# Performance work log

Hardware: AMD Instinct MI355X
Metric: run time of the kernel (lower is better)

The kernel has to match this reference:

```python
import jax, jax.numpy as jnp
import numpy as np

HEADS = 4
DIM_HEAD = 64
SCALE = DIM_HEAD ** -0.5


def setup_inputs() -> dict:
    key = jax.random.key(0)
    k1, k2, k3 = jax.random.split(key, 3)
    C = 256
    hidden = HEADS * DIM_HEAD  # 256
    x = jax.random.normal(k1, (16, C, 64, 64), dtype=jnp.float32)
    # 1x1 conv weights collapsed to [out, in] matrices
    w_qkv = jax.random.normal(k2, (3 * hidden, C), dtype=jnp.float32) * (C ** -0.5)
    w_out = jax.random.normal(k3, (C, hidden), dtype=jnp.float32) * (hidden ** -0.5)
    b_out = jnp.zeros((C,), dtype=jnp.float32)
    return {"x": x, "w_qkv": w_qkv, "w_out": w_out, "b_out": b_out}


def reference(x, w_qkv, w_out, b_out):
    b, c, h, w = x.shape
    n = h * w
    # 1x1 conv == channel GEMM
    qkv = jnp.einsum('bchw,oc->bohw', x, w_qkv)           # [b, 3*hidden, h, w]
    qkv = qkv.reshape(b, 3, HEADS, DIM_HEAD, n)            # [b, 3, H, d, n]
    q, k, v = qkv[:, 0], qkv[:, 1], qkv[:, 2]              # each [b, H, d, n]
    q = jax.nn.softmax(q, axis=2) * SCALE                  # softmax over d
    k = jax.nn.softmax(k, axis=3)                          # softmax over n
    context = jnp.einsum('bhdn,bhen->bhde', k, v)          # [b, H, d, e]
    out = jnp.einsum('bhde,bhdn->bhen', context, q)        # [b, H, e, n]
    out = out.reshape(b, HEADS * DIM_HEAD, h, w)           # [b, hidden, h, w]
    return jnp.einsum('bchw,oc->bohw', out, w_out) + b_out[None, :, None, None]
```

## Files before the change

### kernel.cpp

```cpp
#include <hip/hip_runtime.h>

#define NPIX 4096
#define SCALE 0.125f

typedef _Float16 half8 __attribute__((ext_vector_type(8)));
typedef _Float16 half4 __attribute__((ext_vector_type(4)));
typedef float floatx4 __attribute__((ext_vector_type(4)));

__device__ __forceinline__ void async16(void* lds, const void* g) {
  __builtin_amdgcn_global_load_lds(
      (const __attribute__((address_space(1))) unsigned int*)(uintptr_t)g,
      (__attribute__((address_space(3))) unsigned int*)(unsigned)(uintptr_t)lds,
      16, 0, 0);
}

__global__ __launch_bounds__(256) void split16_kernel(const float* __restrict__ w,
                                                      _Float16* __restrict__ hi,
                                                      _Float16* __restrict__ lo, int n) {
  int i = blockIdx.x * 256 + threadIdx.x;
  if (i < n) {
    float v = w[i];
    _Float16 h = (_Float16)v;
    hi[i] = h;
    lo[i] = (_Float16)(v - (float)h);
  }
}

__global__ __launch_bounds__(256) void transpose16_kernel(const float* __restrict__ x,
                                                          _Float16* __restrict__ xt) {
  __shared__ float t[64][65];
  const int n0 = blockIdx.x * 64, c0 = blockIdx.y * 64, b = blockIdx.z;
  const float* xp = x + (long)b * 256 * NPIX;
  const int tid = threadIdx.x;
  const int r = tid >> 4, c4 = (tid & 15) * 4;
#pragma unroll
  for (int p = 0; p < 4; p++) {
    float4 v = *(const float4*)&xp[(long)(c0 + r + p * 16) * NPIX + n0 + c4];
    t[r + p * 16][c4 + 0] = v.x;
    t[r + p * 16][c4 + 1] = v.y;
    t[r + p * 16][c4 + 2] = v.z;
    t[r + p * 16][c4 + 3] = v.w;
  }
  __syncthreads();
  const int n = tid >> 2, cg = (tid & 3) * 16;
  alignas(16) _Float16 o[16];
#pragma unroll
  for (int i = 0; i < 16; i++) o[i] = (_Float16)t[cg + i][n];
  _Float16* dst = &xt[((long)b * NPIX + n0 + n) * 256 + c0 + cg];
  *(float4*)dst = *(float4*)&o[0];
  *(float4*)(dst + 8) = *(float4*)&o[8];
}

__global__ __launch_bounds__(256) void q_gemm_softmax(const _Float16* __restrict__ Ahp,
                                                      const _Float16* __restrict__ Alp,
                                                      const _Float16* __restrict__ Bt,
                                                      _Float16* __restrict__ PT) {
  union alignas(16) QU {
    _Float16 st[2][3][128 * 32];
    _Float16 pt[128][128];
  };
  __shared__ QU u;
  const int tid = threadIdx.x;
  const int n0 = blockIdx.x * 128, m0 = blockIdx.y * 128;
  const int bz = blockIdx.z;
  const _Float16* Bp = Bt + (long)bz * NPIX * 256;
  const int wv = tid >> 6, l = tid & 63;
  const int r16 = l & 15, q = l >> 4;
  const int mb = (wv >> 1) * 64, nb = (wv & 1) * 64;
  const int r1 = tid >> 2;
  const int o1 = ((tid & 3) * 8) ^ (((r1 >> 1) & 3) * 8);
  const int r2 = r1 + 64;
  const int ldsc1 = (wv * 64) * 8;
  const int ldsc2 = (256 + wv * 64) * 8;
  const int q8 = (q * 8) ^ (((r16 >> 1) & 3) * 8);

  auto STAGE = [&](int buf, int kt) {
    const int k0 = kt * 32;
    async16(&u.st[buf][0][ldsc1], &Ahp[(long)(m0 + r1) * 256 + k0 + o1]);
    async16(&u.st[buf][0][ldsc2], &Ahp[(long)(m0 + r2) * 256 + k0 + o1]);
    async16(&u.st[buf][1][ldsc1], &Alp[(long)(m0 + r1) * 256 + k0 + o1]);
    async16(&u.st[buf][1][ldsc2], &Alp[(long)(m0 + r2) * 256 + k0 + o1]);
    async16(&u.st[buf][2][ldsc1], &Bp[(long)(n0 + r1) * 256 + k0 + o1]);
    async16(&u.st[buf][2][ldsc2], &Bp[(long)(n0 + r2) * 256 + k0 + o1]);
  };

  floatx4 acc[4][4];
#pragma unroll
  for (int i = 0; i < 4; i++)
#pragma unroll
    for (int j = 0; j < 4; j++) acc[i][j] = (floatx4){0.f, 0.f, 0.f, 0.f};

  STAGE(0, 0);
  __syncthreads();
  int cur = 0;
  for (int kt = 0; kt < 8; kt++) {
    if (kt < 7) STAGE(cur ^ 1, kt + 1);
    half8 fa[4], flo[4], fb[4];
#pragma unroll
    for (int i = 0; i < 4; i++) {
      fa[i] = *(const half8*)&u.st[cur][0][(mb + i * 16 + r16) * 32 + q8];
      flo[i] = *(const half8*)&u.st[cur][1][(mb + i * 16 + r16) * 32 + q8];
      fb[i] = *(const half8*)&u.st[cur][2][(nb + i * 16 + r16) * 32 + q8];
    }
#pragma unroll
    for (int i = 0; i < 4; i++)
#pragma unroll
      for (int j = 0; j < 4; j++) {
        acc[i][j] = __builtin_amdgcn_mfma_f32_16x16x32_f16(fa[i], fb[j], acc[i][j], 0, 0, 0);
        acc[i][j] = __builtin_amdgcn_mfma_f32_16x16x32_f16(flo[i], fb[j], acc[i][j], 0, 0, 0);
      }
    __syncthreads();
    cur ^= 1;
  }

#pragma unroll
  for (int j = 0; j < 4; j++) {
    float s = 0.f;
#pragma unroll
    for (int i = 0; i < 4; i++)
#pragma unroll
      for (int t = 0; t < 4; t++) {
        float e = __expf(acc[i][j][t]);
        acc[i][j][t] = e;
        s += e;
      }
    s += __shfl_xor(s, 16, 64);
    s += __shfl_xor(s, 32, 64);
    const float rinv = 1.0f / s;
    const int nl = nb + j * 16 + r16;
    const int swz = (nl & 7) * 8;
#pragma unroll
    for (int i = 0; i < 4; i++) {
      half4 h4;
#pragma unroll
      for (int t = 0; t < 4; t++) h4[t] = (_Float16)(acc[i][j][t] * rinv);
      *(half4*)&u.pt[nl][(mb + i * 16 + q * 4) ^ swz] = h4;
    }
  }
  __syncthreads();
  const int rbase = tid >> 4, c16 = tid & 15;
  _Float16* dst = PT + ((long)(bz * 2 + (m0 >> 7)) * NPIX + n0) * 128;
#pragma unroll
  for (int k = 0; k < 8; k++) {
    const int row = rbase + k * 16;
    const int chunk = c16 ^ (row & 7);
    float4 v = *(const float4*)&u.pt[row][chunk * 8];
    *(float4*)&dst[(long)row * 128 + c16 * 8] = v;
  }
}

#define CPB 2
__global__ __launch_bounds__(256) void kv_ctx_gemm(const _Float16* __restrict__ Ahp,
                                                   const _Float16* __restrict__ Alp,
                                                   const _Float16* __restrict__ Bt,
                                                   float* __restrict__ pbuf,
                                                   float* __restrict__ rsbuf) {
  union alignas(16) KVU {
    _Float16 st[2][3][128 * 32];
    _Float16 ev[128][136];
  };
  __shared__ KVU u;
  const int tid = threadIdx.x;
  const int cg = blockIdx.x;
  const int hi = blockIdx.y;
  const int b = blockIdx.z;
  const _Float16* Bp = Bt + (long)b * NPIX * 256;
  const int wv = tid >> 6, l = tid & 63;
  const int r16 = l & 15, q = l >> 4;
  const int mb = (wv >> 1) * 64, nb = (wv & 1) * 64;
  const int r1 = tid >> 2;
  const int o1 = ((tid & 3) * 8) ^ (((r1 >> 1) & 3) * 8);
  const int ldsc1 = (wv * 64) * 8;
  const int ldsc2 = (256 + wv * 64) * 8;
  const int q8 = (q * 8) ^ (((r16 >> 1) & 3) * 8);
  const long gAk = (long)(256 + hi * 64 + r1) * 256;
  const long gAv = (long)(512 + hi * 64 + r1) * 256;

  auto STAGE = [&](int buf, int kt, int n0) {
    const int k0 = kt * 32;
    async16(&u.st[buf][0][ldsc1], &Ahp[gAk + k0 + o1]);
    async16(&u.st[buf][0][ldsc2], &Ahp[gAv + k0 + o1]);
    async16(&u.st[buf][1][ldsc1], &Alp[gAk + k0 + o1]);
    async16(&u.st[buf][1][ldsc2], &Alp[gAv + k0 + o1]);
    async16(&u.st[buf][2][ldsc1], &Bp[(long)(n0 + r1) * 256 + k0 + o1]);
    async16(&u.st[buf][2][ldsc2], &Bp[(long)(n0 + 64 + r1) * 256 + k0 + o1]);
  };

  floatx4 c2[4];
#pragma unroll
  for (int j = 0; j < 4; j++) c2[j] = (floatx4){0.f, 0.f, 0.f, 0.f};
  float rs = 0.f;

  for (int cs = 0; cs < CPB; cs++) {
    const int n0 = (cg * CPB + cs) * 128;
    floatx4 acc[4][4];
#pragma unroll
    for (int i = 0; i < 4; i++)
#pragma unroll
      for (int j = 0; j < 4; j++) acc[i][j] = (floatx4){0.f, 0.f, 0.f, 0.f};

    STAGE(0, 0, n0);
    __syncthreads();
    int cur = 0;
    for (int kt = 0; kt < 8; kt++) {
      if (kt < 7) STAGE(cur ^ 1, kt + 1, n0);
      half8 fa[4], flo[4], fb[4];
#pragma unroll
      for (int i = 0; i < 4; i++) {
        fa[i] = *(const half8*)&u.st[cur][0][(mb + i * 16 + r16) * 32 + q8];
        flo[i] = *(const half8*)&u.st[cur][1][(mb + i * 16 + r16) * 32 + q8];
        fb[i] = *(const half8*)&u.st[cur][2][(nb + i * 16 + r16) * 32 + q8];
      }
#pragma unroll
      for (int i = 0; i < 4; i++)
#pragma unroll
        for (int j = 0; j < 4; j++) {
          acc[i][j] = __builtin_amdgcn_mfma_f32_16x16x32_f16(fa[i], fb[j], acc[i][j], 0, 0, 0);
          acc[i][j] = __builtin_amdgcn_mfma_f32_16x16x32_f16(flo[i], fb[j], acc[i][j], 0, 0, 0);
        }
      __syncthreads();
      cur ^= 1;
    }

    const bool is_k = (mb == 0);
#pragma unroll
    for (int i = 0; i < 4; i++) {
      const int row = mb + i * 16 + q * 4;
#pragma unroll
      for (int j = 0; j < 4; j++) {
        const int col = nb + j * 16 + r16;
#pragma unroll
        for (int t = 0; t < 4; t++) {
          const float vv0 = acc[i][j][t];
          u.ev[row + t][col] = (_Float16)(is_k ? __expf(vv0) : vv0);
        }
      }
    }
    __syncthreads();

#pragma unroll
    for (int ks = 0; ks < 4; ks++) {
      half8 a = *(const half8*)&u.ev[wv * 16 + r16][ks * 32 + q * 8];
#pragma unroll
      for (int ii = 0; ii < 8; ii++) rs += (float)a[ii];
#pragma unroll
      for (int j = 0; j < 4; j++) {
        half8 bv = *(const half8*)&u.ev[64 + j * 16 + r16][ks * 32 + q * 8];
        c2[j] = __builtin_amdgcn_mfma_f32_16x16x32_f16(a, bv, c2[j], 0, 0, 0);
      }
    }
    __syncthreads();
  }

  rs += __shfl_xor(rs, 16, 64);
  rs += __shfl_xor(rs, 32, 64);
  const int bh = b * 4 + hi;
  float* pp = pbuf + ((long)bh * 16 + cg) * 4096;
#pragma unroll
  for (int j = 0; j < 4; j++)
#pragma unroll
    for (int reg = 0; reg < 4; reg++)
      pp[(wv * 16 + q * 4 + reg) * 64 + j * 16 + r16] = c2[j][reg];
  if (l < 16) rsbuf[((long)bh * 16 + cg) * 64 + wv * 16 + r16] = rs;
}

__global__ __launch_bounds__(256) void reduce_ctx(const float* __restrict__ pbuf,
                                                  float* __restrict__ ctx) {
  int g = blockIdx.x * 256 + threadIdx.x;
  int bh = g >> 12, e = g & 4095;
  const float* pp = pbuf + ((long)bh * 16) * 4096 + e;
  float s = 0.f;
#pragma unroll
  for (int c = 0; c < 16; c++) s += pp[(long)c * 4096];
  ctx[g] = s;
}

__global__ __launch_bounds__(256) void zinv_kernel(const float* __restrict__ rsbuf,
                                                   float* __restrict__ kinvz) {
  int g = blockIdx.x * 256 + threadIdx.x;
  int bh = g >> 6, d = g & 63;
  const float* rp = rsbuf + (long)bh * 16 * 64 + d;
  float s = 0.f;
#pragma unroll
  for (int c = 0; c < 16; c++) s += rp[c * 64];
  kinvz[g] = 1.0f / s;
}

__global__ __launch_bounds__(256) void mctx_kernel(const float* __restrict__ w_out,
                                                   const float* __restrict__ ctx,
                                                   const float* __restrict__ kinvz,
                                                   _Float16* __restrict__ Mhi,
                                                   _Float16* __restrict__ Mlo) {
  __shared__ float sctxT[64][65];
  const int cq = blockIdx.x, h = blockIdx.y, b = blockIdx.z;
  const int bh = b * 4 + h;
  const float* cp = ctx + (long)bh * 4096;
  const int tid = threadIdx.x;
  {
    const int d = tid >> 2, e0 = (tid & 3) * 16;
#pragma unroll
    for (int k = 0; k < 4; k++) {
      float4 v = *(const float4*)&cp[d * 64 + e0 + k * 4];
      sctxT[e0 + k * 4 + 0][d] = v.x;
      sctxT[e0 + k * 4 + 1][d] = v.y;
      sctxT[e0 + k * 4 + 2][d] = v.z;
      sctxT[e0 + k * 4 + 3][d] = v.w;
    }
  }
  __syncthreads();
  const int c = cq * 64 + (tid >> 2);
  const int d0 = (tid & 3) * 16;
  const float* wp = w_out + (long)c * 256 + h * 64;
  float acc[16];
#pragma unroll
  for (int i = 0; i < 16; i++) acc[i] = 0.f;
#pragma unroll
  for (int e4 = 0; e4 < 16; e4++) {
    float4 wv = *(const float4*)&wp[e4 * 4];
#pragma unroll
    for (int u2 = 0; u2 < 4; u2++) {
      const float we = ((const float*)&wv)[u2];
      const int e = e4 * 4 + u2;
#pragma unroll
      for (int dd = 0; dd < 16; dd++) acc[dd] = fmaf(we, sctxT[e][d0 + dd], acc[dd]);
    }
  }
  alignas(16) _Float16 hi16[16], lo16[16];
#pragma unroll
  for (int k4 = 0; k4 < 4; k4++) {
    float4 zv = *(const float4*)&kinvz[bh * 64 + d0 + k4 * 4];
#pragma unroll
    for (int u2 = 0; u2 < 4; u2++) {
      const int dd = k4 * 4 + u2;
      float v = acc[dd] * (SCALE * ((const float*)&zv)[u2]);
      _Float16 hh = (_Float16)v;
      hi16[dd] = hh;
      lo16[dd] = (_Float16)(v - (float)hh);
    }
  }
  _Float16* mh = Mhi + ((long)b * 256 + c) * 256 + h * 64 + d0;
  _Float16* ml = Mlo + ((long)b * 256 + c) * 256 + h * 64 + d0;
#pragma unroll
  for (int k = 0; k < 2; k++) {
    *(float4*)&mh[k * 8] = *(float4*)&hi16[k * 8];
    *(float4*)&ml[k * 8] = *(float4*)&lo16[k * 8];
  }
}

__global__ __launch_bounds__(256) void out_gemm(const _Float16* __restrict__ Mhi,
                                                const _Float16* __restrict__ Mlo,
                                                const _Float16* __restrict__ PT,
                                                float* __restrict__ C,
                                                const float* __restrict__ bias) {
  __shared__ _Float16 st[2][3][128 * 32];
  const int tid = threadIdx.x;
  const int n0 = blockIdx.x * 128, m0 = blockIdx.y * 128;
  const int b = blockIdx.z;
  const _Float16* Ah = Mhi + (long)b * 65536;
  const _Float16* Al = Mlo + (long)b * 65536;
  float* Cp = C + (long)b * 256 * NPIX;
  const int wv = tid >> 6, l = tid & 63;
  const int r16 = l & 15, q = l >> 4;
  const int mb = (wv >> 1) * 64, nb = (wv & 1) * 64;
  const int r1 = tid >> 2;
  const int o1 = ((tid & 3) * 8) ^ (((r1 >> 1) & 3) * 8);
  const int r2 = r1 + 64;
  const int ldsc1 = (wv * 64) * 8;
  const int ldsc2 = (256 + wv * 64) * 8;
  const int q8 = (q * 8) ^ (((r16 >> 1) & 3) * 8);

  auto STAGE = [&](int buf, int kt) {
    const int k0 = kt * 32;
    async16(&st[buf][0][ldsc1], &Ah[(long)(m0 + r1) * 256 + k0 + o1]);
    async16(&st[buf][0][ldsc2], &Ah[(long)(m0 + r2) * 256 + k0 + o1]);
    async16(&st[buf][1][ldsc1], &Al[(long)(m0 + r1) * 256 + k0 + o1]);
    async16(&st[buf][1][ldsc2], &Al[(long)(m0 + r2) * 256 + k0 + o1]);
    const _Float16* Bk = PT + ((long)(b * 2 + (kt >> 2)) * NPIX + n0) * 128;
    async16(&st[buf][2][ldsc1], &Bk[(long)r1 * 128 + (kt & 3) * 32 + o1]);
    async16(&st[buf][2][ldsc2], &Bk[(long)(r1 + 64) * 128 + (kt & 3) * 32 + o1]);
  };

  floatx4 acc[4][4];
#pragma unroll
  for (int i = 0; i < 4; i++)
#pragma unroll
    for (int j = 0; j < 4; j++) acc[i][j] = (floatx4){0.f, 0.f, 0.f, 0.f};

  STAGE(0, 0);
  __syncthreads();
  int cur = 0;
  for (int kt = 0; kt < 8; kt++) {
    if (kt < 7) STAGE(cur ^ 1, kt + 1);
    half8 fa[4], flo[4], fb[4];
#pragma unroll
    for (int i = 0; i < 4; i++) {
      fa[i] = *(const half8*)&st[cur][0][(mb + i * 16 + r16) * 32 + q8];
      flo[i] = *(const half8*)&st[cur][1][(mb + i * 16 + r16) * 32 + q8];
      fb[i] = *(const half8*)&st[cur][2][(nb + i * 16 + r16) * 32 + q8];
    }
#pragma unroll
    for (int i = 0; i < 4; i++)
#pragma unroll
      for (int j = 0; j < 4; j++) {
        acc[i][j] = __builtin_amdgcn_mfma_f32_16x16x32_f16(fa[i], fb[j], acc[i][j], 0, 0, 0);
        acc[i][j] = __builtin_amdgcn_mfma_f32_16x16x32_f16(flo[i], fb[j], acc[i][j], 0, 0, 0);
      }
    __syncthreads();
    cur ^= 1;
  }
#pragma unroll
  for (int i = 0; i < 4; i++) {
    const int mrow = m0 + mb + i * 16 + q * 4;
#pragma unroll
    for (int t = 0; t < 4; t++) {
      float bz = bias[mrow + t];
#pragma unroll
      for (int j = 0; j < 4; j++) {
        Cp[(long)(mrow + t) * NPIX + n0 + nb + j * 16 + r16] = acc[i][j][t] + bz;
      }
    }
  }
}

extern "C" void kernel_launch(void* const* d_in, const int* in_sizes, int n_in,
                              void* d_out, int out_size, void* d_ws, size_t ws_size,
                              hipStream_t stream) {
  const float* x = (const float*)d_in[0];
  const float* w_qkv = (const float*)d_in[1];
  const float* w_out = (const float*)d_in[2];
  const float* b_out = (const float*)d_in[3];
  float* out = (float*)d_out;

  _Float16* PT = (_Float16*)d_ws;
  float* ctx = (float*)(PT + (long)16 * 2 * NPIX * 128);
  float* kinvz = ctx + 64 * 4096;
  float* rsbuf = kinvz + 4096;
  _Float16* wq_hi = (_Float16*)(rsbuf + 64 * 16 * 64);
  _Float16* wq_lo = wq_hi + 768 * 256;
  _Float16* Mhi = wq_lo + 768 * 256;
  _Float16* Mlo = Mhi + 16 * 256 * 256;
  _Float16* xt = (_Float16*)d_out;
  float* pbuf = (float*)d_out + (1 << 23);

  split16_kernel<<<768, 256, 0, stream>>>(w_qkv, wq_hi, wq_lo, 768 * 256);
  transpose16_kernel<<<dim3(64, 4, 16), 256, 0, stream>>>(x, xt);
  kv_ctx_gemm<<<dim3(16, 4, 16), 256, 0, stream>>>(wq_hi, wq_lo, xt, pbuf, rsbuf);
  reduce_ctx<<<1024, 256, 0, stream>>>(pbuf, ctx);
  zinv_kernel<<<16, 256, 0, stream>>>(rsbuf, kinvz);
  q_gemm_softmax<<<dim3(32, 2, 16), 256, 0, stream>>>(wq_hi, wq_lo, xt, PT);
  mctx_kernel<<<dim3(4, 4, 16), 256, 0, stream>>>(w_out, ctx, kinvz, Mhi, Mlo);
  out_gemm<<<dim3(32, 2, 16), 256, 0, stream>>>(Mhi, Mlo, PT, out, b_out);
}
```

Before: 222.2 us.

## Drop lo-split in K/V GEMM and fuse context reductions into mctx kernel

The K/V projection GEMM now uses only the fp16 high part of the weights, removing the second MFMA pass and the staging of the low-part weights. This halves MFMA work and cuts LDS traffic in that kernel, at the cost of lower precision in K and V. The partial-context reduction and the softmax-denominator reduction are folded into the mctx kernel, which removes two small launches and the ctx/kinvz intermediate buffers. Each mctx block now reads its 16 partial context slices redundantly (the same data for each of its 4 column groups), and the launch order is changed so mctx runs before the Q GEMM.

```diff
diff --git a/kernel.cpp b/kernel.cpp
--- a/kernel.cpp
+++ b/kernel.cpp
@@ -151,12 +151,11 @@
 
 #define CPB 2
 __global__ __launch_bounds__(256) void kv_ctx_gemm(const _Float16* __restrict__ Ahp,
-                                                   const _Float16* __restrict__ Alp,
                                                    const _Float16* __restrict__ Bt,
                                                    float* __restrict__ pbuf,
                                                    float* __restrict__ rsbuf) {
   union alignas(16) KVU {
-    _Float16 st[2][3][128 * 32];
+    _Float16 st[2][2][128 * 32];
     _Float16 ev[128][136];
   };
   __shared__ KVU u;
@@ -180,10 +179,8 @@
     const int k0 = kt * 32;
     async16(&u.st[buf][0][ldsc1], &Ahp[gAk + k0 + o1]);
     async16(&u.st[buf][0][ldsc2], &Ahp[gAv + k0 + o1]);
-    async16(&u.st[buf][1][ldsc1], &Alp[gAk + k0 + o1]);
-    async16(&u.st[buf][1][ldsc2], &Alp[gAv + k0 + o1]);
-    async16(&u.st[buf][2][ldsc1], &Bp[(long)(n0 + r1) * 256 + k0 + o1]);
-    async16(&u.st[buf][2][ldsc2], &Bp[(long)(n0 + 64 + r1) * 256 + k0 + o1]);
+    async16(&u.st[buf][1][ldsc1], &Bp[(long)(n0 + r1) * 256 + k0 + o1]);
+    async16(&u.st[buf][1][ldsc2], &Bp[(long)(n0 + 64 + r1) * 256 + k0 + o1]);
   };
 
   floatx4 c2[4];
@@ -204,19 +201,17 @@
     int cur = 0;
     for (int kt = 0; kt < 8; kt++) {
       if (kt < 7) STAGE(cur ^ 1, kt + 1, n0);
-      half8 fa[4], flo[4], fb[4];
+      half8 fa[4], fb[4];
 #pragma unroll
       for (int i = 0; i < 4; i++) {
         fa[i] = *(const half8*)&u.st[cur][0][(mb + i * 16 + r16) * 32 + q8];
-        flo[i] = *(const half8*)&u.st[cur][1][(mb + i * 16 + r16) * 32 + q8];
-        fb[i] = *(const half8*)&u.st[cur][2][(nb + i * 16 + r16) * 32 + q8];
+        fb[i] = *(const half8*)&u.st[cur][1][(nb + i * 16 + r16) * 32 + q8];
       }
 #pragma unroll
       for (int i = 0; i < 4; i++)
 #pragma unroll
         for (int j = 0; j < 4; j++) {
           acc[i][j] = __builtin_amdgcn_mfma_f32_16x16x32_f16(fa[i], fb[j], acc[i][j], 0, 0, 0);
-          acc[i][j] = __builtin_amdgcn_mfma_f32_16x16x32_f16(flo[i], fb[j], acc[i][j], 0, 0, 0);
         }
       __syncthreads();
       cur ^= 1;
@@ -264,48 +259,41 @@
   if (l < 16) rsbuf[((long)bh * 16 + cg) * 64 + wv * 16 + r16] = rs;
 }
 
-__global__ __launch_bounds__(256) void reduce_ctx(const float* __restrict__ pbuf,
-                                                  float* __restrict__ ctx) {
-  int g = blockIdx.x * 256 + threadIdx.x;
-  int bh = g >> 12, e = g & 4095;
-  const float* pp = pbuf + ((long)bh * 16) * 4096 + e;
-  float s = 0.f;
-#pragma unroll
-  for (int c = 0; c < 16; c++) s += pp[(long)c * 4096];
-  ctx[g] = s;
-}
-
-__global__ __launch_bounds__(256) void zinv_kernel(const float* __restrict__ rsbuf,
-                                                   float* __restrict__ kinvz) {
-  int g = blockIdx.x * 256 + threadIdx.x;
-  int bh = g >> 6, d = g & 63;
-  const float* rp = rsbuf + (long)bh * 16 * 64 + d;
-  float s = 0.f;
-#pragma unroll
-  for (int c = 0; c < 16; c++) s += rp[c * 64];
-  kinvz[g] = 1.0f / s;
-}
-
-__global__ __launch_bounds__(256) void mctx_kernel(const float* __restrict__ w_out,
-                                                   const float* __restrict__ ctx,
-                                                   const float* __restrict__ kinvz,
-                                                   _Float16* __restrict__ Mhi,
-                                                   _Float16* __restrict__ Mlo) {
+__global__ __launch_bounds__(256) void mctx_fused(const float* __restrict__ w_out,
+                                                  const float* __restrict__ pbuf,
+                                                  const float* __restrict__ rsbuf,
+                                                  _Float16* __restrict__ Mhi,
+                                                  _Float16* __restrict__ Mlo) {
   __shared__ float sctxT[64][65];
+  __shared__ float sinv[64];
   const int cq = blockIdx.x, h = blockIdx.y, b = blockIdx.z;
   const int bh = b * 4 + h;
-  const float* cp = ctx + (long)bh * 4096;
+  const float* pp = pbuf + (long)bh * 16 * 4096;
   const int tid = threadIdx.x;
   {
     const int d = tid >> 2, e0 = (tid & 3) * 16;
-#pragma unroll
-    for (int k = 0; k < 4; k++) {
-      float4 v = *(const float4*)&cp[d * 64 + e0 + k * 4];
-      sctxT[e0 + k * 4 + 0][d] = v.x;
-      sctxT[e0 + k * 4 + 1][d] = v.y;
-      sctxT[e0 + k * 4 + 2][d] = v.z;
-      sctxT[e0 + k * 4 + 3][d] = v.w;
-    }
+    float s0[16];
+#pragma unroll
+    for (int i = 0; i < 16; i++) s0[i] = 0.f;
+    for (int c = 0; c < 16; c++) {
+#pragma unroll
+      for (int k = 0; k < 4; k++) {
+        float4 v = *(const float4*)&pp[(long)c * 4096 + d * 64 + e0 + k * 4];
+        s0[k * 4 + 0] += v.x;
+        s0[k * 4 + 1] += v.y;
+        s0[k * 4 + 2] += v.z;
+        s0[k * 4 + 3] += v.w;
+      }
+    }
+#pragma unroll
+    for (int i = 0; i < 16; i++) sctxT[e0 + i][d] = s0[i];
+  }
+  if (tid < 64) {
+    const float* rp = rsbuf + (long)bh * 16 * 64 + tid;
+    float z = 0.f;
+#pragma unroll
+    for (int c = 0; c < 16; c++) z += rp[c * 64];
+    sinv[tid] = 1.0f / z;
   }
   __syncthreads();
   const int c = cq * 64 + (tid >> 2);
@@ -328,7 +316,7 @@
   alignas(16) _Float16 hi16[16], lo16[16];
 #pragma unroll
   for (int k4 = 0; k4 < 4; k4++) {
-    float4 zv = *(const float4*)&kinvz[bh * 64 + d0 + k4 * 4];
+    float4 zv = *(const float4*)&sinv[d0 + k4 * 4];
 #pragma unroll
     for (int u2 = 0; u2 < 4; u2++) {
       const int dd = k4 * 4 + u2;
@@ -432,9 +420,7 @@
   float* out = (float*)d_out;
 
   _Float16* PT = (_Float16*)d_ws;
-  float* ctx = (float*)(PT + (long)16 * 2 * NPIX * 128);
-  float* kinvz = ctx + 64 * 4096;
-  float* rsbuf = kinvz + 4096;
+  float* rsbuf = (float*)(PT + (long)16 * 2 * NPIX * 128);
   _Float16* wq_hi = (_Float16*)(rsbuf + 64 * 16 * 64);
   _Float16* wq_lo = wq_hi + 768 * 256;
   _Float16* Mhi = wq_lo + 768 * 256;
@@ -444,10 +430,8 @@
 
   split16_kernel<<<768, 256, 0, stream>>>(w_qkv, wq_hi, wq_lo, 768 * 256);
   transpose16_kernel<<<dim3(64, 4, 16), 256, 0, stream>>>(x, xt);
-  kv_ctx_gemm<<<dim3(16, 4, 16), 256, 0, stream>>>(wq_hi, wq_lo, xt, pbuf, rsbuf);
-  reduce_ctx<<<1024, 256, 0, stream>>>(pbuf, ctx);
-  zinv_kernel<<<16, 256, 0, stream>>>(rsbuf, kinvz);
+  kv_ctx_gemm<<<dim3(16, 4, 16), 256, 0, stream>>>(wq_hi, xt, pbuf, rsbuf);
+  mctx_fused<<<dim3(4, 4, 16), 256, 0, stream>>>(w_out, pbuf, rsbuf, Mhi, Mlo);
   q_gemm_softmax<<<dim3(32, 2, 16), 256, 0, stream>>>(wq_hi, wq_lo, xt, PT);
-  mctx_kernel<<<dim3(4, 4, 16), 256, 0, stream>>>(w_out, ctx, kinvz, Mhi, Mlo);
   out_gemm<<<dim3(32, 2, 16), 256, 0, stream>>>(Mhi, Mlo, PT, out, b_out);
 }
```

New measurement: 208.4 us. 6.2% less time.
